# Performance work log

Measured on AMD Instinct MI355X. Metric: run time of the kernel, lower is better.

The kernel has to match this reference:

```python
import jax, jax.numpy as jnp
import numpy as np

B, NQ, NK, D_IN, HD = 1, 16384, 7933, 1024, 512
R = 0.3  # keep-top-r fraction used for the quantile threshold


def _l2norm(x):
    # matches F.normalize(p=2, dim=-1, eps=1e-12)
    n = jnp.linalg.norm(x, axis=-1, keepdims=True)
    return x / jnp.maximum(n, 1e-12)


def setup_inputs() -> dict:
    key = jax.random.key(0)
    ks = jax.random.split(key, 10)
    s = 0.02
    return {
        "query": jax.random.normal(ks[0], (B, NQ, D_IN), jnp.float32),
        "key_x": jax.random.normal(ks[1], (B, NK, D_IN), jnp.float32),
        "wq_w": jax.random.normal(ks[2], (HD, D_IN), jnp.float32) * s,
        "wq_b": jnp.zeros((HD,), jnp.float32),
        "wk_w": jax.random.normal(ks[3], (HD, D_IN), jnp.float32) * s,
        "wk_b": jnp.zeros((HD,), jnp.float32),
        "wa_w": jax.random.normal(ks[4], (1, NK), jnp.float32) * s,
        "wa_b": jnp.zeros((1,), jnp.float32),
        "cls_w": jax.random.normal(ks[5], (1, HD), jnp.float32) * s,
        "cls_b": jnp.zeros((1,), jnp.float32),
    }


def reference(query, key_x, wq_w, wq_b, wk_w, wk_b, wa_w, wa_b, cls_w, cls_b):
    # WQ / WK: Linear + Tanh
    q = jnp.tanh(jnp.einsum("bnd,hd->bnh", query, wq_w) + wq_b)   # [B,NQ,HD]
    k = jnp.tanh(jnp.einsum("bnd,hd->bnh", key_x, wk_w) + wk_b)   # [B,NK,HD]
    # normalized dot-product scores
    A = jnp.einsum("bqh,bkh->bqk", _l2norm(q), _l2norm(k))        # [B,NQ,NK]
    # WA: Linear(NK -> 1)
    A1 = jnp.einsum("bqk,ok->bqo", A, wa_w) + wa_b                # [B,NQ,1]
    # quantile threshold from batch 0 (torch: sorted ascending, index -int(r*NQ))
    thre = jax.lax.stop_gradient(jnp.sort(A1[0, :, 0])[-int(R * NQ)])
    A1 = jnp.where(A1 > thre, A1, 0.0)                            # F.threshold(., thre, 0)
    attn = jax.nn.softmax(A1, axis=1)                             # softmax over NQ (zeros included)
    attn_t = jnp.transpose(attn, (0, 2, 1))                       # [B,1,NQ]
    z = jnp.matmul(attn_t, q).reshape(-1, HD)                     # [B,HD]
    y_prob = z @ cls_w.T + cls_b                                  # [B,1]
    return (y_prob, attn_t)
```

## Files before the change

kernel.cpp:

```cpp
#include <hip/hip_runtime.h>
#include <math.h>

#define NQ 16384
#define NK 7933
#define DI 1024
#define HD 512
#define RANK_TARGET 11469

typedef __bf16 bf16x8 __attribute__((ext_vector_type(8)));
typedef float  f32x4  __attribute__((ext_vector_type(4)));

#define GLOAD_LDS16(g, l)                                                     \
  __builtin_amdgcn_global_load_lds(                                           \
      (const __attribute__((address_space(1))) void*)(g),                     \
      (__attribute__((address_space(3))) void*)(l), 16, 0, 0)

__device__ __forceinline__ unsigned mapf(float f) {
  unsigned b = __float_as_uint(f);
  return (b & 0x80000000u) ? ~b : (b | 0x80000000u);
}

__device__ __forceinline__ bf16x8 cvt8(float4 a, float4 b) {
  bf16x8 o;
  o[0] = (__bf16)a.x; o[1] = (__bf16)a.y; o[2] = (__bf16)a.z; o[3] = (__bf16)a.w;
  o[4] = (__bf16)b.x; o[5] = (__bf16)b.y; o[6] = (__bf16)b.z; o[7] = (__bf16)b.w;
  return o;
}

__global__ void conv_w(const float* __restrict__ wq, const float* __restrict__ wk,
                       __bf16* __restrict__ wqbf, __bf16* __restrict__ wkbf,
                       unsigned* __restrict__ zero_region) {
  if (blockIdx.x == 0) {
    for (int j = threadIdx.x; j < 1088; j += 256) zero_region[j] = 0u;
  }
  const int W8 = HD * DI / 8;
  int i = blockIdx.x * 256 + threadIdx.x;
  const float* s; __bf16* d; int j;
  if (i < W8) { s = wq; d = wqbf; j = i; }
  else        { s = wk; d = wkbf; j = i - W8; }
  float4 a = ((const float4*)s)[2 * j];
  float4 b = ((const float4*)s)[2 * j + 1];
  bf16x8 o;
  o[0] = (__bf16)a.x; o[1] = (__bf16)a.y; o[2] = (__bf16)a.z; o[3] = (__bf16)a.w;
  o[4] = (__bf16)b.x; o[5] = (__bf16)b.y; o[6] = (__bf16)b.z; o[7] = (__bf16)b.w;
  ((bf16x8*)d)[j] = o;
}

template <bool FUSE_A1>
__global__ __launch_bounds__(512, 4)
void gemm_f32a_tanh(const float* __restrict__ A, const __bf16* __restrict__ B,
                    const float* __restrict__ bias, float* __restrict__ C, int M,
                    const float* __restrict__ v, float* __restrict__ A1dot,
                    float* __restrict__ A1ss) {
  constexpr int K = DI;
  constexpr int N = HD;
  __shared__ __align__(16) __bf16 sA[2][64 * 64];
  __shared__ __align__(16) __bf16 sB[2][256 * 64];

  const int tid  = threadIdx.x;
  const int lane = tid & 63;
  const int wave = tid >> 6;
  const int wr = wave >> 2;
  const int wc = wave & 3;
  const int m0 = blockIdx.x * 64, n0 = blockIdx.y * 256;

  const int arow = tid >> 3;
  const int acb  = tid & 7;
  const int aoff = arow * 64 + ((acb ^ (arow & 7)) << 3);
  int ga = m0 + arow; if (ga > M - 1) ga = M - 1;
  const float* ap = A + (size_t)ga * K + acb * 8;

  const int srow = lane >> 3;
  const int scol = ((lane & 7) ^ srow) << 3;

  const int lrow = lane & 15;
  const int chi  = lane >> 4;

  f32x4 acc[2][4] = {};

  {
    float4 x0 = *(const float4*)(ap);
    float4 x1 = *(const float4*)(ap + 4);
#pragma unroll
    for (int c = 0; c < 4; ++c) {
      int seg = wave * 4 + c;
      GLOAD_LDS16(B + (size_t)(n0 + seg * 8 + srow) * K + scol, &sB[0][seg * 512]);
    }
    *(bf16x8*)&sA[0][aoff] = cvt8(x0, x1);
    __syncthreads();
  }

  int buf = 0;
  for (int t = 0; t < 16; ++t) {
    const int kk = t * 64;
    float4 x0, x1;
    if (t < 15) {
      x0 = *(const float4*)(ap + kk + 64);
      x1 = *(const float4*)(ap + kk + 68);
#pragma unroll
      for (int c = 0; c < 4; ++c) {
        int seg = wave * 4 + c;
        GLOAD_LDS16(B + (size_t)(n0 + seg * 8 + srow) * K + kk + 64 + scol,
                    &sB[buf ^ 1][seg * 512]);
      }
    }
    const __bf16* sAc = sA[buf];
    const __bf16* sBc = sB[buf];
#pragma unroll
    for (int ks = 0; ks < 64; ks += 32) {
      const int cc = (ks >> 3) + chi;
      const int sw = ((cc ^ (lrow & 7)) << 3);
      bf16x8 af[2], bfr[4];
      af[0] = *(const bf16x8*)(&sAc[(wr * 32 + lrow) * 64 + sw]);
      af[1] = *(const bf16x8*)(&sAc[(wr * 32 + 16 + lrow) * 64 + sw]);
#pragma unroll
      for (int ni = 0; ni < 4; ++ni)
        bfr[ni] = *(const bf16x8*)(&sBc[(wc * 64 + ni * 16 + lrow) * 64 + sw]);
#pragma unroll
      for (int ni = 0; ni < 4; ++ni) {
        acc[0][ni] = __builtin_amdgcn_mfma_f32_16x16x32_bf16(af[0], bfr[ni], acc[0][ni], 0, 0, 0);
        acc[1][ni] = __builtin_amdgcn_mfma_f32_16x16x32_bf16(af[1], bfr[ni], acc[1][ni], 0, 0, 0);
      }
    }
    if (t < 15) {
      *(bf16x8*)&sA[buf ^ 1][aoff] = cvt8(x0, x1);
      __syncthreads();
      buf ^= 1;
    }
  }

  const int rbase = m0 + wr * 32 + ((lane >> 4) << 2);
  const int cbase = n0 + wc * 64 + (lane & 15);
  float b4[4], v4[4];
#pragma unroll
  for (int ni = 0; ni < 4; ++ni) {
    b4[ni] = bias[cbase + ni * 16];
    if constexpr (FUSE_A1) v4[ni] = v[cbase + ni * 16];
  }
#pragma unroll
  for (int mi = 0; mi < 2; ++mi) {
#pragma unroll
    for (int r = 0; r < 4; ++r) {
      int grow = rbase + mi * 16 + r;
      if (grow < M) {
        float pd = 0.f, pss = 0.f;
#pragma unroll
        for (int ni = 0; ni < 4; ++ni) {
          float val = tanhf(acc[mi][ni][r] + b4[ni]);
          C[(size_t)grow * N + cbase + ni * 16] = val;
          if constexpr (FUSE_A1) { pd += val * v4[ni]; pss += val * val; }
        }
        if constexpr (FUSE_A1) {
#pragma unroll
          for (int off = 1; off < 16; off <<= 1) {
            pd += __shfl_xor(pd, off);
            pss += __shfl_xor(pss, off);
          }
          if ((lane & 15) == 0) {
            atomicAdd(&A1dot[grow], pd);
            atomicAdd(&A1ss[grow], pss);
          }
        }
      }
    }
  }
}

__global__ __launch_bounds__(256)
void reduce_v_zero(const float* __restrict__ kt, const float* __restrict__ wa,
                   float* __restrict__ v, int M, uint2* __restrict__ zr) {
  {
    int g = blockIdx.x * 256 + threadIdx.x;
    uint2 zz; zz.x = 0u; zz.y = 0u;
    zr[g] = zz;
    if (g < 24576 - 16384) zr[16384 + g] = zz;
  }
  __shared__ float vpart[4][512];
  const int tid = threadIdx.x, lane = tid & 63, wave = tid >> 6;
  const int gw = blockIdx.x * 4 + wave;
  const int tw = gridDim.x * 4;
  float acc[8] = {0, 0, 0, 0, 0, 0, 0, 0};
  for (int r = gw; r < M; r += tw) {
    const float4* p = (const float4*)(kt + (size_t)r * HD + lane * 8);
    float4 x = p[0], y = p[1];
    float ss = x.x * x.x + x.y * x.y + x.z * x.z + x.w * x.w
             + y.x * y.x + y.y * y.y + y.z * y.z + y.w * y.w;
#pragma unroll
    for (int off = 32; off; off >>= 1) ss += __shfl_xor(ss, off);
    float s = wa[r] / fmaxf(sqrtf(ss), 1e-12f);
    acc[0] += s * x.x; acc[1] += s * x.y; acc[2] += s * x.z; acc[3] += s * x.w;
    acc[4] += s * y.x; acc[5] += s * y.y; acc[6] += s * y.z; acc[7] += s * y.w;
  }
#pragma unroll
  for (int j = 0; j < 8; ++j) vpart[wave][lane * 8 + j] = acc[j];
  __syncthreads();
  for (int c = tid; c < 512; c += 256)
    atomicAdd(&v[c], vpart[0][c] + vpart[1][c] + vpart[2][c] + vpart[3][c]);
}

__global__ __launch_bounds__(1024)
void select_kernel(const float* __restrict__ A1dot, const float* __restrict__ A1ss,
                   const float* __restrict__ wa_b, float* __restrict__ A1,
                   unsigned* __restrict__ keyg, float* __restrict__ scf) {
  __shared__ unsigned wred1[16], wred2[16], wred3[16];
  __shared__ unsigned s_res;
  const int t = threadIdx.x, lane = t & 63, wave = t >> 6;
  const float wab = wa_b[0];
  unsigned kloc[16];
#pragma unroll 4
  for (int j = 0; j < 16; ++j) {
    int i = j * 1024 + t;
    float d = A1dot[i], ss = A1ss[i];
    float a1 = d / fmaxf(sqrtf(ss), 1e-12f) + wab;
    A1[i] = a1;
    unsigned k = mapf(a1);
    kloc[j] = k;
    keyg[i] = k;
  }
  if (t == 0) s_res = 0u;
  __syncthreads();

  for (int b = 30; b >= 0; b -= 2) {
    const unsigned res = s_res;
    const unsigned t1 = res | (1u << b);
    const unsigned t2 = res | (2u << b);
    const unsigned t3 = res | (3u << b);
    unsigned c1 = 0, c2 = 0, c3 = 0;
#pragma unroll
    for (int j = 0; j < 16; ++j) {
      unsigned k = kloc[j];
      c1 += (k < t1); c2 += (k < t2); c3 += (k < t3);
    }
#pragma unroll
    for (int off = 32; off; off >>= 1) {
      c1 += __shfl_xor(c1, off);
      c2 += __shfl_xor(c2, off);
      c3 += __shfl_xor(c3, off);
    }
    if (lane == 0) { wred1[wave] = c1; wred2[wave] = c2; wred3[wave] = c3; }
    __syncthreads();
    if (t == 0) {
      unsigned C1 = 0, C2 = 0, C3 = 0;
      for (int w = 0; w < 16; ++w) { C1 += wred1[w]; C2 += wred2[w]; C3 += wred3[w]; }
      unsigned nr = res;
      if (C3 <= RANK_TARGET)      nr = t3;
      else if (C2 <= RANK_TARGET) nr = t2;
      else if (C1 <= RANK_TARGET) nr = t1;
      s_res = nr;
    }
    __syncthreads();
  }
  if (t == 0) {
    unsigned key = s_res;
    unsigned bits = (key & 0x80000000u) ? (key ^ 0x80000000u) : ~key;
    scf[0] = __uint_as_float(bits);
  }
}

__global__ __launch_bounds__(256)
void expz(const float* __restrict__ A1, const float* __restrict__ qt,
          float* __restrict__ scf, float* __restrict__ e_out,
          float* __restrict__ z) {
  __shared__ float vpart[4][512];
  __shared__ float esum[4];
  const int tid = threadIdx.x, lane = tid & 63, wave = tid >> 6;
  const float thre = scf[0];
  const int gw = blockIdx.x * 4 + wave;
  const int tw = gridDim.x * 4;
  float acc[8] = {0, 0, 0, 0, 0, 0, 0, 0};
  float es = 0.f;
  for (int r = gw; r < NQ; r += tw) {
    float x = A1[r]; x = (x > thre) ? x : 0.f;
    float e = expf(x - thre);
    if (lane == 0) e_out[r] = e;
    es += e;
    const float4* p = (const float4*)(qt + (size_t)r * HD + lane * 8);
    float4 u = p[0], w = p[1];
    acc[0] += e * u.x; acc[1] += e * u.y; acc[2] += e * u.z; acc[3] += e * u.w;
    acc[4] += e * w.x; acc[5] += e * w.y; acc[6] += e * w.z; acc[7] += e * w.w;
  }
  if (lane == 0) esum[wave] = es;
#pragma unroll
  for (int j = 0; j < 8; ++j) vpart[wave][lane * 8 + j] = acc[j];
  __syncthreads();
  for (int c = tid; c < 512; c += 256)
    atomicAdd(&z[c], vpart[0][c] + vpart[1][c] + vpart[2][c] + vpart[3][c]);
  if (tid == 0) atomicAdd(&scf[2], esum[0] + esum[1] + esum[2] + esum[3]);
}

__global__ __launch_bounds__(256)
void finalize(float* __restrict__ attn, const float* __restrict__ scf,
              const float* __restrict__ z, const float* __restrict__ cls_w,
              const float* __restrict__ cls_b, float* __restrict__ y) {
  const float invZ = 1.f / scf[2];
  if (blockIdx.x < 64) {
    int i = blockIdx.x * 256 + threadIdx.x;
    attn[i] *= invZ;
  } else if (threadIdx.x < 64) {
    const int lane = threadIdx.x;
    const float4* zp = (const float4*)(z + lane * 8);
    const float4* wp = (const float4*)(cls_w + lane * 8);
    float4 a = zp[0], b = zp[1], c = wp[0], d = wp[1];
    float dot = a.x * c.x + a.y * c.y + a.z * c.z + a.w * c.w
              + b.x * d.x + b.y * d.y + b.z * d.z + b.w * d.w;
#pragma unroll
    for (int off = 32; off; off >>= 1) dot += __shfl_xor(dot, off);
    if (lane == 0) y[0] = dot * invZ + cls_b[0];
  }
}

#define OFF_WQBF 0u
#define OFF_WKBF 1048576u
#define OFF_A1D  1048576u
#define OFF_A1S  1114112u
#define OFF_KEY  1179648u
#define OFF_A1   35651584u
#define OFF_V    35717120u
#define OFF_Z    35719168u
#define OFF_SC   35721216u
#define OFF_KT   51968256u
#define OFF_QT   35721472u

extern "C" void kernel_launch(void* const* d_in, const int* in_sizes, int n_in,
                              void* d_out, int out_size, void* d_ws, size_t ws_size,
                              hipStream_t stream) {
  const float* query = (const float*)d_in[0];
  const float* key_x = (const float*)d_in[1];
  const float* wq_w  = (const float*)d_in[2];
  const float* wq_b  = (const float*)d_in[3];
  const float* wk_w  = (const float*)d_in[4];
  const float* wk_b  = (const float*)d_in[5];
  const float* wa_w  = (const float*)d_in[6];
  const float* wa_b  = (const float*)d_in[7];
  const float* cls_w = (const float*)d_in[8];
  const float* cls_b = (const float*)d_in[9];
  float* out = (float*)d_out;

  char* ws = (char*)d_ws;
  __bf16* wqbf  = (__bf16*)(ws + OFF_WQBF);
  __bf16* wkbf  = (__bf16*)(ws + OFF_WKBF);
  float*  A1dot = (float*)(ws + OFF_A1D);
  float*  A1ss  = (float*)(ws + OFF_A1S);
  unsigned* keyg = (unsigned*)(ws + OFF_KEY);
  float*  A1    = (float*)(ws + OFF_A1);
  float*  v     = (float*)(ws + OFF_V);
  float*  z     = (float*)(ws + OFF_Z);
  float*  scf   = (float*)(ws + OFF_SC);
  float*  ktanh = (float*)(ws + OFF_KT);
  float*  qtanh = (float*)(ws + OFF_QT);
  float*  out_attn = out + 1;

  conv_w<<<512, 256, 0, stream>>>(wq_w, wk_w, wqbf, wkbf, (unsigned*)v);

  gemm_f32a_tanh<false><<<dim3(124, 2), 512, 0, stream>>>(
      key_x, wkbf, wk_b, ktanh, NK, nullptr, nullptr, nullptr);

  reduce_v_zero<<<64, 256, 0, stream>>>(ktanh, wa_w, v, NK, (uint2*)A1dot);

  gemm_f32a_tanh<true><<<dim3(256, 2), 512, 0, stream>>>(
      query, wqbf, wq_b, qtanh, NQ, v, A1dot, A1ss);

  select_kernel<<<1, 1024, 0, stream>>>(A1dot, A1ss, wa_b, A1, keyg, scf);

  expz<<<256, 256, 0, stream>>>(A1, qtanh, scf, out_attn, z);

  finalize<<<65, 256, 0, stream>>>(out_attn, scf, z, cls_w, cls_b, out);
}
```

Before: 258.6 us.

## Pre-convert GEMM A operands to bf16 and overlap query conversion with key GEMM

Activations (key_x and query) are now converted to bf16 in workspace up front: key_x in the weight-conversion kernel, and query in spare blocks that run alongside the key GEMM in one launch. Both GEMMs can then stream A tiles into LDS with direct global-to-LDS loads, the same way they load B, instead of loading fp32 into registers, converting and storing to LDS inside the main loop. The cost is extra global traffic: writing and re-reading bf16 copies of both activations. The reduce_v launch also gets a larger grid.

```diff
diff --git a/kernel.cpp b/kernel.cpp
--- a/kernel.cpp
+++ b/kernel.cpp
@@ -27,48 +27,43 @@
   return o;
 }
 
-__global__ void conv_w(const float* __restrict__ wq, const float* __restrict__ wk,
-                       __bf16* __restrict__ wqbf, __bf16* __restrict__ wkbf,
-                       unsigned* __restrict__ zero_region) {
+__global__ void conv_wk(const float* __restrict__ wq, const float* __restrict__ wk,
+                        const float* __restrict__ key,
+                        __bf16* __restrict__ wqbf, __bf16* __restrict__ wkbf,
+                        __bf16* __restrict__ kbf, unsigned* __restrict__ zero_region) {
   if (blockIdx.x == 0) {
     for (int j = threadIdx.x; j < 1088; j += 256) zero_region[j] = 0u;
   }
-  const int W8 = HD * DI / 8;
-  int i = blockIdx.x * 256 + threadIdx.x;
-  const float* s; __bf16* d; int j;
-  if (i < W8) { s = wq; d = wqbf; j = i; }
-  else        { s = wk; d = wkbf; j = i - W8; }
-  float4 a = ((const float4*)s)[2 * j];
-  float4 b = ((const float4*)s)[2 * j + 1];
-  bf16x8 o;
-  o[0] = (__bf16)a.x; o[1] = (__bf16)a.y; o[2] = (__bf16)a.z; o[3] = (__bf16)a.w;
-  o[4] = (__bf16)b.x; o[5] = (__bf16)b.y; o[6] = (__bf16)b.z; o[7] = (__bf16)b.w;
-  ((bf16x8*)d)[j] = o;
+  const int NK8 = NK * DI / 8;
+  const int W8  = HD * DI / 8;
+  const int total = NK8 + 2 * W8;
+  int i = blockIdx.x * blockDim.x + threadIdx.x;
+  int stride = gridDim.x * blockDim.x;
+  for (; i < total; i += stride) {
+    const float* s; __bf16* d; int j;
+    if (i < NK8)            { s = key; d = kbf;  j = i; }
+    else if (i < NK8 + W8)  { s = wq;  d = wqbf; j = i - NK8; }
+    else                    { s = wk;  d = wkbf; j = i - NK8 - W8; }
+    float4 a = ((const float4*)s)[2 * j];
+    float4 b = ((const float4*)s)[2 * j + 1];
+    ((bf16x8*)d)[j] = cvt8(a, b);
+  }
 }
 
 template <bool FUSE_A1>
-__global__ __launch_bounds__(512, 4)
-void gemm_f32a_tanh(const float* __restrict__ A, const __bf16* __restrict__ B,
-                    const float* __restrict__ bias, float* __restrict__ C, int M,
-                    const float* __restrict__ v, float* __restrict__ A1dot,
-                    float* __restrict__ A1ss) {
+__device__ __forceinline__ void gemm_core(
+    const __bf16* __restrict__ A, const __bf16* __restrict__ B,
+    const float* __restrict__ bias, float* __restrict__ C, int M,
+    int m0, int n0, __bf16* sA, __bf16* sB,
+    const float* __restrict__ v, float* __restrict__ A1dot,
+    float* __restrict__ A1ss) {
   constexpr int K = DI;
   constexpr int N = HD;
-  __shared__ __align__(16) __bf16 sA[2][64 * 64];
-  __shared__ __align__(16) __bf16 sB[2][256 * 64];
-
   const int tid  = threadIdx.x;
   const int lane = tid & 63;
   const int wave = tid >> 6;
   const int wr = wave >> 2;
   const int wc = wave & 3;
-  const int m0 = blockIdx.x * 64, n0 = blockIdx.y * 256;
-
-  const int arow = tid >> 3;
-  const int acb  = tid & 7;
-  const int aoff = arow * 64 + ((acb ^ (arow & 7)) << 3);
-  int ga = m0 + arow; if (ga > M - 1) ga = M - 1;
-  const float* ap = A + (size_t)ga * K + acb * 8;
 
   const int srow = lane >> 3;
   const int scol = ((lane & 7) ^ srow) << 3;
@@ -76,36 +71,35 @@
   const int lrow = lane & 15;
   const int chi  = lane >> 4;
 
+  int gaA = m0 + wave * 8 + srow; if (gaA > M - 1) gaA = M - 1;
+  const __bf16* Ap = A + (size_t)gaA * K + scol;
+  const __bf16* Bp0 = B + (size_t)(n0 + (wave * 4 + 0) * 8 + srow) * K + scol;
+  const __bf16* Bp1 = B + (size_t)(n0 + (wave * 4 + 1) * 8 + srow) * K + scol;
+  const __bf16* Bp2 = B + (size_t)(n0 + (wave * 4 + 2) * 8 + srow) * K + scol;
+  const __bf16* Bp3 = B + (size_t)(n0 + (wave * 4 + 3) * 8 + srow) * K + scol;
+
   f32x4 acc[2][4] = {};
 
-  {
-    float4 x0 = *(const float4*)(ap);
-    float4 x1 = *(const float4*)(ap + 4);
-#pragma unroll
-    for (int c = 0; c < 4; ++c) {
-      int seg = wave * 4 + c;
-      GLOAD_LDS16(B + (size_t)(n0 + seg * 8 + srow) * K + scol, &sB[0][seg * 512]);
-    }
-    *(bf16x8*)&sA[0][aoff] = cvt8(x0, x1);
-    __syncthreads();
-  }
+  GLOAD_LDS16(Ap, &sA[wave * 512]);
+  GLOAD_LDS16(Bp0, &sB[(wave * 4 + 0) * 512]);
+  GLOAD_LDS16(Bp1, &sB[(wave * 4 + 1) * 512]);
+  GLOAD_LDS16(Bp2, &sB[(wave * 4 + 2) * 512]);
+  GLOAD_LDS16(Bp3, &sB[(wave * 4 + 3) * 512]);
+  __syncthreads();
 
   int buf = 0;
   for (int t = 0; t < 16; ++t) {
     const int kk = t * 64;
-    float4 x0, x1;
     if (t < 15) {
-      x0 = *(const float4*)(ap + kk + 64);
-      x1 = *(const float4*)(ap + kk + 68);
-#pragma unroll
-      for (int c = 0; c < 4; ++c) {
-        int seg = wave * 4 + c;
-        GLOAD_LDS16(B + (size_t)(n0 + seg * 8 + srow) * K + kk + 64 + scol,
-                    &sB[buf ^ 1][seg * 512]);
-      }
-    }
-    const __bf16* sAc = sA[buf];
-    const __bf16* sBc = sB[buf];
+      const int ob = (buf ^ 1);
+      GLOAD_LDS16(Ap + kk + 64, &sA[ob * 4096 + wave * 512]);
+      GLOAD_LDS16(Bp0 + kk + 64, &sB[ob * 16384 + (wave * 4 + 0) * 512]);
+      GLOAD_LDS16(Bp1 + kk + 64, &sB[ob * 16384 + (wave * 4 + 1) * 512]);
+      GLOAD_LDS16(Bp2 + kk + 64, &sB[ob * 16384 + (wave * 4 + 2) * 512]);
+      GLOAD_LDS16(Bp3 + kk + 64, &sB[ob * 16384 + (wave * 4 + 3) * 512]);
+    }
+    const __bf16* sAc = sA + buf * 4096;
+    const __bf16* sBc = sB + buf * 16384;
 #pragma unroll
     for (int ks = 0; ks < 64; ks += 32) {
       const int cc = (ks >> 3) + chi;
@@ -123,7 +117,6 @@
       }
     }
     if (t < 15) {
-      *(bf16x8*)&sA[buf ^ 1][aoff] = cvt8(x0, x1);
       __syncthreads();
       buf ^= 1;
     }
@@ -166,14 +159,46 @@
   }
 }
 
+__global__ __launch_bounds__(512, 4)
+void gemm_k_conv_q(const __bf16* __restrict__ kbf, const __bf16* __restrict__ wkbf,
+                   const float* __restrict__ wk_b, float* __restrict__ ktanh,
+                   const float* __restrict__ query, __bf16* __restrict__ qbf) {
+  __shared__ __align__(16) __bf16 sA[2 * 64 * 64];
+  __shared__ __align__(16) __bf16 sB[2 * 256 * 64];
+  const int bid = blockIdx.x;
+  if (bid < 248) {
+    const int m0 = (bid >> 1) * 64;
+    const int n0 = (bid & 1) * 256;
+    gemm_core<false>(kbf, wkbf, wk_b, ktanh, NK, m0, n0, sA, sB,
+                     nullptr, nullptr, nullptr);
+  } else {
+    const int total = NQ * DI / 8;
+    for (int i = (bid - 248) * 512 + threadIdx.x; i < total; i += 264 * 512) {
+      float4 a = ((const float4*)query)[2 * i];
+      float4 b = ((const float4*)query)[2 * i + 1];
+      ((bf16x8*)qbf)[i] = cvt8(a, b);
+    }
+  }
+}
+
+__global__ __launch_bounds__(512, 4)
+void gemm_q(const __bf16* __restrict__ qbf, const __bf16* __restrict__ wqbf,
+            const float* __restrict__ wq_b, float* __restrict__ qtanh,
+            const float* __restrict__ v, float* __restrict__ A1dot,
+            float* __restrict__ A1ss) {
+  __shared__ __align__(16) __bf16 sA[2 * 64 * 64];
+  __shared__ __align__(16) __bf16 sB[2 * 256 * 64];
+  gemm_core<true>(qbf, wqbf, wq_b, qtanh, NQ, blockIdx.x * 64, blockIdx.y * 256,
+                  sA, sB, v, A1dot, A1ss);
+}
+
 __global__ __launch_bounds__(256)
 void reduce_v_zero(const float* __restrict__ kt, const float* __restrict__ wa,
                    float* __restrict__ v, int M, uint2* __restrict__ zr) {
   {
     int g = blockIdx.x * 256 + threadIdx.x;
     uint2 zz; zz.x = 0u; zz.y = 0u;
-    zr[g] = zz;
-    if (g < 24576 - 16384) zr[16384 + g] = zz;
+    if (g < 24576) zr[g] = zz;
   }
   __shared__ float vpart[4][512];
   const int tid = threadIdx.x, lane = tid & 63, wave = tid >> 6;
@@ -314,10 +339,12 @@
 #define OFF_A1D  1048576u
 #define OFF_A1S  1114112u
 #define OFF_KEY  1179648u
+#define OFF_QBF  2097152u
 #define OFF_A1   35651584u
 #define OFF_V    35717120u
 #define OFF_Z    35719168u
 #define OFF_SC   35721216u
+#define OFF_KBF  35721472u
 #define OFF_KT   51968256u
 #define OFF_QT   35721472u
 
@@ -342,23 +369,24 @@
   float*  A1dot = (float*)(ws + OFF_A1D);
   float*  A1ss  = (float*)(ws + OFF_A1S);
   unsigned* keyg = (unsigned*)(ws + OFF_KEY);
+  __bf16* qbf   = (__bf16*)(ws + OFF_QBF);
   float*  A1    = (float*)(ws + OFF_A1);
   float*  v     = (float*)(ws + OFF_V);
   float*  z     = (float*)(ws + OFF_Z);
   float*  scf   = (float*)(ws + OFF_SC);
+  __bf16* kbf   = (__bf16*)(ws + OFF_KBF);
   float*  ktanh = (float*)(ws + OFF_KT);
   float*  qtanh = (float*)(ws + OFF_QT);
   float*  out_attn = out + 1;
 
-  conv_w<<<512, 256, 0, stream>>>(wq_w, wk_w, wqbf, wkbf, (unsigned*)v);
-
-  gemm_f32a_tanh<false><<<dim3(124, 2), 512, 0, stream>>>(
-      key_x, wkbf, wk_b, ktanh, NK, nullptr, nullptr, nullptr);
-
-  reduce_v_zero<<<64, 256, 0, stream>>>(ktanh, wa_w, v, NK, (uint2*)A1dot);
-
-  gemm_f32a_tanh<true><<<dim3(256, 2), 512, 0, stream>>>(
-      query, wqbf, wq_b, qtanh, NQ, v, A1dot, A1ss);
+  conv_wk<<<2048, 256, 0, stream>>>(wq_w, wk_w, key_x, wqbf, wkbf, kbf,
+                                    (unsigned*)v);
+
+  gemm_k_conv_q<<<512, 512, 0, stream>>>(kbf, wkbf, wk_b, ktanh, query, qbf);
+
+  reduce_v_zero<<<256, 256, 0, stream>>>(ktanh, wa_w, v, NK, (uint2*)A1dot);
+
+  gemm_q<<<dim3(256, 2), 512, 0, stream>>>(qbf, wqbf, wq_b, qtanh, v, A1dot, A1ss);
 
   select_kernel<<<1, 1024, 0, stream>>>(A1dot, A1ss, wa_b, A1, keyg, scf);
 
```

Measured after the change: 256.8 us. No clear change (-0.7%).
